# Performance work log

Hardware: AMD Instinct MI355X
Metric: run time of the kernel (lower is better)

Reference implementation:

```python
import jax, jax.numpy as jnp
import numpy as np

B = 8192
N_INPUTS = 16 * 12 * 64  # 12288, FEATURE_FACTORIZE=False
H0, H1, H2 = 256, 32, 32
OUTPUT_SCALE = 300.0
WDL_SCALE = 200.0
AVG_ACTIVE = 30.0  # ~30 active features per position (NNUE sparsity)


def setup_inputs() -> dict:
    key = jax.random.key(0)
    ks = jax.random.split(key, 11)
    p = AVG_ACTIVE / N_INPUTS
    # near-one-hot sparse binary feature vectors, as produced by get_features()
    wf = (jax.random.uniform(ks[0], (B, N_INPUTS)) < p).astype(jnp.float32)
    bf = (jax.random.uniform(ks[1], (B, N_INPUTS)) < p).astype(jnp.float32)
    side = jax.random.randint(ks[2], (B,), 0, 2).astype(jnp.bool_)
    qs1, qs2, qs3 = float(1 << 6), float(1 << 6), float(1 << 5)
    ft_w = jax.random.normal(ks[3], (H0, N_INPUTS), jnp.float32) * jnp.sqrt(2.0 / N_INPUTS)
    ft_b = jax.random.normal(ks[4], (H0,), jnp.float32) * 0.5
    l1_w = jax.random.normal(ks[5], (H1, 2 * H0), jnp.float32) * (32.0 / qs1)
    l1_b = jax.random.normal(ks[6], (H1,), jnp.float32) * 0.5
    l2_w = jax.random.normal(ks[7], (H2, H1), jnp.float32) * (32.0 / qs2)
    l2_b = jax.random.normal(ks[8], (H2,), jnp.float32) * 0.5
    l3_w = jax.random.normal(ks[9], (1, H2), jnp.float32) * (2048.0 / (OUTPUT_SCALE * qs3))
    l3_b = jax.random.normal(ks[10], (1,), jnp.float32) * 0.5
    return {"white_features": wf, "black_features": bf, "side": side,
            "ft_w": ft_w, "ft_b": ft_b, "l1_w": l1_w, "l1_b": l1_b,
            "l2_w": l2_w, "l2_b": l2_b, "l3_w": l3_w, "l3_b": l3_b}


def reference(white_features, black_features, side, ft_w, ft_b,
              l1_w, l1_b, l2_w, l2_b, l3_w, l3_b):
    # feature transformer on each perspective: [B, H0]
    w = white_features @ ft_w.T + ft_b
    b = black_features @ ft_w.T + ft_b
    s = side[:, None]
    # side-to-move perspective first: [B, 2*H0]
    acc = jnp.where(s, jnp.concatenate([w, b], axis=1),
                    jnp.concatenate([b, w], axis=1))
    o0 = jnp.clip(acc, 0.0, 1.0)
    o1 = jnp.clip(o0 @ l1_w.T + l1_b, 0.0, 1.0)
    o2 = jnp.clip(o1 @ l2_w.T + l2_b, 0.0, 1.0)
    o3 = (o2 @ l3_w.T + l3_b) * OUTPUT_SCALE  # [B, 1]
    return jax.nn.sigmoid(o3 / WDL_SCALE)
```

## Files before the change

kernel.cpp:

```cpp
#include <hip/hip_runtime.h>
#include <math.h>

#define NB 8192
#define NI 12288
#define H0 256
#define H1 32
#define H2 32
#define MAXA 256
#define OUT_SCALE 300.0f
#define WDL_SCALE 200.0f

typedef float f32x4 __attribute__((ext_vector_type(4)));

__global__ __launch_bounds__(256) void nnue_ft_transpose(
    const float* __restrict__ src, float* __restrict__ dst)
{
    __shared__ float tile[64][65];
    const int bx = blockIdx.x;
    const int by = blockIdx.y;
    const int tx = threadIdx.x;
    const int ty = threadIdx.y;
    const int col = bx * 64 + tx;
    for (int j = ty; j < 64; j += 4)
        tile[j][tx] = src[(size_t)(by * 64 + j) * NI + col];
    __syncthreads();
    const int h = by * 64 + tx;
    for (int j = ty; j < 64; j += 4)
        dst[(size_t)(bx * 64 + j) * H0 + h] = tile[tx][j];
}

__global__ __launch_bounds__(256) void nnue_fwd(
    const float* __restrict__ wf, const float* __restrict__ bf,
    const int* __restrict__ side,
    const float* __restrict__ ft,
    const float* __restrict__ ft_b,
    const float* __restrict__ l1_w, const float* __restrict__ l1_b,
    const float* __restrict__ l2_w, const float* __restrict__ l2_b,
    const float* __restrict__ l3_w, const float* __restrict__ l3_b,
    float* __restrict__ out, int tflag)
{
    __shared__ int   idxW[MAXA], idxB[MAXA];
    __shared__ int   cnts[2];
    __shared__ float o0[2 * H0];
    __shared__ float o1[H1];

    const int row = blockIdx.x;
    const int t   = threadIdx.x;
    if (t < 2) cnts[t] = 0;
    __syncthreads();

    const f32x4* wf4 = (const f32x4*)(wf + (size_t)row * NI);
    const f32x4* bf4 = (const f32x4*)(bf + (size_t)row * NI);
    const float ftb = ft_b[t];

    {
        f32x4 v[12];
        #pragma unroll
        for (int k = 0; k < 12; ++k)
            v[k] = __builtin_nontemporal_load(&wf4[t + k * 256]);
        #pragma unroll
        for (int k = 0; k < 12; ++k) {
            const int base = (t + k * 256) * 4;
            int m = (v[k].x != 0.f ? 1 : 0) | (v[k].y != 0.f ? 2 : 0)
                  | (v[k].z != 0.f ? 4 : 0) | (v[k].w != 0.f ? 8 : 0);
            while (m) {
                const int b = __ffs(m) - 1;
                m &= m - 1;
                idxW[atomicAdd(&cnts[0], 1)] = base + b;
            }
        }
    }
    {
        f32x4 v[12];
        #pragma unroll
        for (int k = 0; k < 12; ++k)
            v[k] = __builtin_nontemporal_load(&bf4[t + k * 256]);
        #pragma unroll
        for (int k = 0; k < 12; ++k) {
            const int base = (t + k * 256) * 4;
            int m = (v[k].x != 0.f ? 1 : 0) | (v[k].y != 0.f ? 2 : 0)
                  | (v[k].z != 0.f ? 4 : 0) | (v[k].w != 0.f ? 8 : 0);
            while (m) {
                const int b = __ffs(m) - 1;
                m &= m - 1;
                idxB[atomicAdd(&cnts[1], 1)] = base + b;
            }
        }
    }
    __syncthreads();

    const int nW = cnts[0], nB = cnts[1];
    float accW, accB;
    if (tflag) {
        float a0 = 0.f, a1 = 0.f, a2 = 0.f, a3 = 0.f;
        int i = 0;
        for (; i + 4 <= nW; i += 4) {
            const int i0 = __builtin_amdgcn_readfirstlane(idxW[i]);
            const int i1 = __builtin_amdgcn_readfirstlane(idxW[i + 1]);
            const int i2 = __builtin_amdgcn_readfirstlane(idxW[i + 2]);
            const int i3 = __builtin_amdgcn_readfirstlane(idxW[i + 3]);
            a0 += ft[(size_t)i0 * H0 + t];
            a1 += ft[(size_t)i1 * H0 + t];
            a2 += ft[(size_t)i2 * H0 + t];
            a3 += ft[(size_t)i3 * H0 + t];
        }
        for (; i < nW; ++i)
            a0 += ft[(size_t)__builtin_amdgcn_readfirstlane(idxW[i]) * H0 + t];
        accW = ftb + ((a0 + a1) + (a2 + a3));

        float b0 = 0.f, b1 = 0.f, b2 = 0.f, b3 = 0.f;
        i = 0;
        for (; i + 4 <= nB; i += 4) {
            const int i0 = __builtin_amdgcn_readfirstlane(idxB[i]);
            const int i1 = __builtin_amdgcn_readfirstlane(idxB[i + 1]);
            const int i2 = __builtin_amdgcn_readfirstlane(idxB[i + 2]);
            const int i3 = __builtin_amdgcn_readfirstlane(idxB[i + 3]);
            b0 += ft[(size_t)i0 * H0 + t];
            b1 += ft[(size_t)i1 * H0 + t];
            b2 += ft[(size_t)i2 * H0 + t];
            b3 += ft[(size_t)i3 * H0 + t];
        }
        for (; i < nB; ++i)
            b0 += ft[(size_t)__builtin_amdgcn_readfirstlane(idxB[i]) * H0 + t];
        accB = ftb + ((b0 + b1) + (b2 + b3));
    } else {
        accW = ftb; accB = ftb;
        const float* ftr = ft + (size_t)t * NI;
        for (int i = 0; i < nW; ++i) accW += ftr[idxW[i]];
        for (int i = 0; i < nB; ++i) accB += ftr[idxB[i]];
    }

    const bool s = side[row] != 0;
    const float wv = fminf(fmaxf(accW, 0.f), 1.f);
    const float bv = fminf(fmaxf(accB, 0.f), 1.f);
    o0[t]      = s ? wv : bv;
    o0[t + H0] = s ? bv : wv;
    __syncthreads();

    {
        const int j = t >> 3, p = t & 7;
        const float* wrow = l1_w + j * (2 * H0);
        float sum = 0.f;
        #pragma unroll
        for (int m = 0; m < 64; ++m) {
            const int k = p + 8 * m;
            sum += wrow[k] * o0[k];
        }
        sum += __shfl_xor(sum, 1);
        sum += __shfl_xor(sum, 2);
        sum += __shfl_xor(sum, 4);
        if (p == 0) o1[j] = fminf(fmaxf(sum + l1_b[j], 0.f), 1.f);
    }
    __syncthreads();

    if (t < 32) {
        const float* wrow = l2_w + t * H1;
        float sum2 = 0.f;
        #pragma unroll
        for (int k = 0; k < H1; ++k) sum2 += wrow[k] * o1[k];
        const float o2v = fminf(fmaxf(sum2 + l2_b[t], 0.f), 1.f);
        float part = o2v * l3_w[t];
        part += __shfl_xor(part, 1);
        part += __shfl_xor(part, 2);
        part += __shfl_xor(part, 4);
        part += __shfl_xor(part, 8);
        part += __shfl_xor(part, 16);
        if (t == 0) {
            const float o3 = (part + l3_b[0]) * OUT_SCALE;
            out[row] = 1.f / (1.f + __expf(-o3 / WDL_SCALE));
        }
    }
}

extern "C" void kernel_launch(void* const* d_in, const int* in_sizes, int n_in,
                              void* d_out, int out_size, void* d_ws, size_t ws_size,
                              hipStream_t stream) {
    const float* wf   = (const float*)d_in[0];
    const float* bf   = (const float*)d_in[1];
    const int*   side = (const int*)d_in[2];
    const float* ft_w = (const float*)d_in[3];
    const float* ft_b = (const float*)d_in[4];
    const float* l1_w = (const float*)d_in[5];
    const float* l1_b = (const float*)d_in[6];
    const float* l2_w = (const float*)d_in[7];
    const float* l2_b = (const float*)d_in[8];
    const float* l3_w = (const float*)d_in[9];
    const float* l3_b = (const float*)d_in[10];
    float*       out  = (float*)d_out;

    const size_t needT = (size_t)NI * H0 * sizeof(float);
    const int tflag = (ws_size >= needT) ? 1 : 0;
    const float* ft = ft_w;
    if (tflag) {
        float* ftT = (float*)d_ws;
        nnue_ft_transpose<<<dim3(NI / 64, H0 / 64), dim3(64, 4), 0, stream>>>(ft_w, ftT);
        ft = ftT;
    }
    nnue_fwd<<<NB, 256, 0, stream>>>(wf, bf, side, ft, ft_b,
                                     l1_w, l1_b, l2_w, l2_b, l3_w, l3_b,
                                     out, tflag);
}
```

Before: 183.4 us.

## Split sparse feature gather across wavefronts with vectorized row loads and LDS reduction

```diff
diff --git a/kernel.cpp b/kernel.cpp
--- a/kernel.cpp
+++ b/kernel.cpp
@@ -41,6 +41,7 @@
 {
     __shared__ int   idxW[MAXA], idxB[MAXA];
     __shared__ int   cnts[2];
+    __shared__ float pacc[4][2][H0] __attribute__((aligned(16)));
     __shared__ float o0[2 * H0];
     __shared__ float o1[H1];
 
@@ -90,46 +91,45 @@
     __syncthreads();
 
     const int nW = cnts[0], nB = cnts[1];
-    float accW, accB;
+    const int w = t >> 6;
+    const int l = t & 63;
+
     if (tflag) {
-        float a0 = 0.f, a1 = 0.f, a2 = 0.f, a3 = 0.f;
-        int i = 0;
-        for (; i + 4 <= nW; i += 4) {
-            const int i0 = __builtin_amdgcn_readfirstlane(idxW[i]);
-            const int i1 = __builtin_amdgcn_readfirstlane(idxW[i + 1]);
-            const int i2 = __builtin_amdgcn_readfirstlane(idxW[i + 2]);
-            const int i3 = __builtin_amdgcn_readfirstlane(idxW[i + 3]);
-            a0 += ft[(size_t)i0 * H0 + t];
-            a1 += ft[(size_t)i1 * H0 + t];
-            a2 += ft[(size_t)i2 * H0 + t];
-            a3 += ft[(size_t)i3 * H0 + t];
-        }
-        for (; i < nW; ++i)
-            a0 += ft[(size_t)__builtin_amdgcn_readfirstlane(idxW[i]) * H0 + t];
-        accW = ftb + ((a0 + a1) + (a2 + a3));
-
-        float b0 = 0.f, b1 = 0.f, b2 = 0.f, b3 = 0.f;
-        i = 0;
-        for (; i + 4 <= nB; i += 4) {
-            const int i0 = __builtin_amdgcn_readfirstlane(idxB[i]);
-            const int i1 = __builtin_amdgcn_readfirstlane(idxB[i + 1]);
-            const int i2 = __builtin_amdgcn_readfirstlane(idxB[i + 2]);
-            const int i3 = __builtin_amdgcn_readfirstlane(idxB[i + 3]);
-            b0 += ft[(size_t)i0 * H0 + t];
-            b1 += ft[(size_t)i1 * H0 + t];
-            b2 += ft[(size_t)i2 * H0 + t];
-            b3 += ft[(size_t)i3 * H0 + t];
-        }
-        for (; i < nB; ++i)
-            b0 += ft[(size_t)__builtin_amdgcn_readfirstlane(idxB[i]) * H0 + t];
-        accB = ftb + ((b0 + b1) + (b2 + b3));
+        f32x4 aw0 = {0.f, 0.f, 0.f, 0.f}, aw1 = {0.f, 0.f, 0.f, 0.f};
+        int i = w;
+        for (; i + 4 < nW; i += 8) {
+            const f32x4 r0 = *(const f32x4*)(ft + (size_t)idxW[i] * H0 + 4 * l);
+            const f32x4 r1 = *(const f32x4*)(ft + (size_t)idxW[i + 4] * H0 + 4 * l);
+            aw0 += r0; aw1 += r1;
+        }
+        if (i < nW)
+            aw0 += *(const f32x4*)(ft + (size_t)idxW[i] * H0 + 4 * l);
+
+        f32x4 ab0 = {0.f, 0.f, 0.f, 0.f}, ab1 = {0.f, 0.f, 0.f, 0.f};
+        i = w;
+        for (; i + 4 < nB; i += 8) {
+            const f32x4 r0 = *(const f32x4*)(ft + (size_t)idxB[i] * H0 + 4 * l);
+            const f32x4 r1 = *(const f32x4*)(ft + (size_t)idxB[i + 4] * H0 + 4 * l);
+            ab0 += r0; ab1 += r1;
+        }
+        if (i < nB)
+            ab0 += *(const f32x4*)(ft + (size_t)idxB[i] * H0 + 4 * l);
+
+        *(f32x4*)&pacc[w][0][4 * l] = aw0 + aw1;
+        *(f32x4*)&pacc[w][1][4 * l] = ab0 + ab1;
     } else {
-        accW = ftb; accB = ftb;
+        float aW = 0.f, aB = 0.f;
         const float* ftr = ft + (size_t)t * NI;
-        for (int i = 0; i < nW; ++i) accW += ftr[idxW[i]];
-        for (int i = 0; i < nB; ++i) accB += ftr[idxB[i]];
-    }
-
+        for (int j = 0; j < nW; ++j) aW += ftr[idxW[j]];
+        for (int j = 0; j < nB; ++j) aB += ftr[idxB[j]];
+        if (w == 0) { pacc[0][0][t % 64] = 0.f; }
+        pacc[0][0][t] = aW; pacc[1][0][t] = 0.f; pacc[2][0][t] = 0.f; pacc[3][0][t] = 0.f;
+        pacc[0][1][t] = aB; pacc[1][1][t] = 0.f; pacc[2][1][t] = 0.f; pacc[3][1][t] = 0.f;
+    }
+    __syncthreads();
+
+    const float accW = ftb + ((pacc[0][0][t] + pacc[1][0][t]) + (pacc[2][0][t] + pacc[3][0][t]));
+    const float accB = ftb + ((pacc[0][1][t] + pacc[1][1][t]) + (pacc[2][1][t] + pacc[3][1][t]));
     const bool s = side[row] != 0;
     const float wv = fminf(fmaxf(accW, 0.f), 1.f);
     const float bv = fminf(fmaxf(accB, 0.f), 1.f);
```

New measurement: 177.3 us. 3.3% less time.

## Process one batch row per wavefront with vectorized gather and transposed dense weights

Applied to the files above, without the earlier changes.

```diff
diff --git a/kernel.cpp b/kernel.cpp
--- a/kernel.cpp
+++ b/kernel.cpp
@@ -11,6 +11,11 @@
 #define WDL_SCALE 200.0f
 
 typedef float f32x4 __attribute__((ext_vector_type(4)));
+
+#define FTT_B  ((size_t)NI * H0 * 4)
+#define L1T_B  ((size_t)2 * H0 * H1 * 4)
+#define L2T_B  ((size_t)H1 * H2 * 4)
+#define WS_NEED (FTT_B + L1T_B + L2T_B)
 
 __global__ __launch_bounds__(256) void nnue_ft_transpose(
     const float* __restrict__ src, float* __restrict__ dst)
@@ -29,7 +34,167 @@
         dst[(size_t)(bx * 64 + j) * H0 + h] = tile[tx][j];
 }
 
-__global__ __launch_bounds__(256) void nnue_fwd(
+__global__ __launch_bounds__(256) void nnue_small_transpose(
+    const float* __restrict__ l1_w, const float* __restrict__ l2_w,
+    float* __restrict__ l1T, float* __restrict__ l2T)
+{
+    const int i = blockIdx.x * 256 + threadIdx.x;
+    if (i < 2 * H0 * H1) {
+        const int k = i >> 5, j = i & 31;
+        l1T[i] = l1_w[j * (2 * H0) + k];
+    }
+    const int i2 = i - 2 * H0 * H1;
+    if (i2 >= 0 && i2 < H1 * H2) {
+        const int k = i2 >> 5, j = i2 & 31;
+        l2T[i2] = l2_w[j * H1 + k];
+    }
+}
+
+__global__ __launch_bounds__(256) void nnue_fwd_wave(
+    const float* __restrict__ wf, const float* __restrict__ bf,
+    const int* __restrict__ side,
+    const float* __restrict__ ft,
+    const float* __restrict__ ft_b,
+    const float* __restrict__ l1T, const float* __restrict__ l1_b,
+    const float* __restrict__ l2T, const float* __restrict__ l2_b,
+    const float* __restrict__ l3_w, const float* __restrict__ l3_b,
+    float* __restrict__ out)
+{
+    __shared__ int   idx[4][2][MAXA];
+    __shared__ int   cnt[4][2];
+    __shared__ float o0s[4][2 * H0];
+    __shared__ float o1s[4][H1];
+
+    const int t = threadIdx.x;
+    const int w = t >> 6;
+    const int l = t & 63;
+    const int row = blockIdx.x * 4 + w;
+
+    if (l == 0) { cnt[w][0] = 0; cnt[w][1] = 0; }
+
+    #pragma unroll 1
+    for (int p = 0; p < 2; ++p) {
+        const float* src = p ? bf : wf;
+        const f32x4* s4 = (const f32x4*)(src + (size_t)row * NI);
+        int* myidx = idx[w][p];
+        int* mycnt = &cnt[w][p];
+
+        auto proc = [&](const f32x4* v, int cbase) {
+            #pragma unroll
+            for (int u = 0; u < 8; ++u) {
+                const int e = cbase * 512 + u * 64 + l;
+                int m = (v[u].x != 0.f ? 1 : 0) | (v[u].y != 0.f ? 2 : 0)
+                      | (v[u].z != 0.f ? 4 : 0) | (v[u].w != 0.f ? 8 : 0);
+                while (m) {
+                    const int b = __ffs(m) - 1;
+                    m &= m - 1;
+                    const int off = atomicAdd(mycnt, 1);
+                    if (off < MAXA) myidx[off] = e * 4 + b;
+                }
+            }
+        };
+
+        f32x4 va[8], vb[8];
+        #pragma unroll
+        for (int u = 0; u < 8; ++u)
+            va[u] = __builtin_nontemporal_load(&s4[u * 64 + l]);
+        #pragma unroll
+        for (int c = 0; c < 6; c += 2) {
+            #pragma unroll
+            for (int u = 0; u < 8; ++u)
+                vb[u] = __builtin_nontemporal_load(&s4[(c + 1) * 512 + u * 64 + l]);
+            proc(va, c);
+            if (c + 2 < 6) {
+                #pragma unroll
+                for (int u = 0; u < 8; ++u)
+                    va[u] = __builtin_nontemporal_load(&s4[(c + 2) * 512 + u * 64 + l]);
+            }
+            proc(vb, c + 1);
+        }
+    }
+
+    const int nW = min(cnt[w][0], MAXA);
+    const int nB = min(cnt[w][1], MAXA);
+    const float* ftl = ft + 4 * l;
+
+    f32x4 a0 = {0.f,0.f,0.f,0.f}, a1 = a0, a2 = a0, a3 = a0;
+    int i = 0;
+    for (; i + 4 <= nW; i += 4) {
+        const int i0 = __builtin_amdgcn_readfirstlane(idx[w][0][i]);
+        const int i1 = __builtin_amdgcn_readfirstlane(idx[w][0][i + 1]);
+        const int i2 = __builtin_amdgcn_readfirstlane(idx[w][0][i + 2]);
+        const int i3 = __builtin_amdgcn_readfirstlane(idx[w][0][i + 3]);
+        a0 += *(const f32x4*)(ftl + (size_t)i0 * H0);
+        a1 += *(const f32x4*)(ftl + (size_t)i1 * H0);
+        a2 += *(const f32x4*)(ftl + (size_t)i2 * H0);
+        a3 += *(const f32x4*)(ftl + (size_t)i3 * H0);
+    }
+    for (; i < nW; ++i)
+        a0 += *(const f32x4*)(ftl + (size_t)__builtin_amdgcn_readfirstlane(idx[w][0][i]) * H0);
+    f32x4 accW = (a0 + a1) + (a2 + a3);
+
+    f32x4 b0 = {0.f,0.f,0.f,0.f}, b1 = b0, b2 = b0, b3 = b0;
+    i = 0;
+    for (; i + 4 <= nB; i += 4) {
+        const int i0 = __builtin_amdgcn_readfirstlane(idx[w][1][i]);
+        const int i1 = __builtin_amdgcn_readfirstlane(idx[w][1][i + 1]);
+        const int i2 = __builtin_amdgcn_readfirstlane(idx[w][1][i + 2]);
+        const int i3 = __builtin_amdgcn_readfirstlane(idx[w][1][i + 3]);
+        b0 += *(const f32x4*)(ftl + (size_t)i0 * H0);
+        b1 += *(const f32x4*)(ftl + (size_t)i1 * H0);
+        b2 += *(const f32x4*)(ftl + (size_t)i2 * H0);
+        b3 += *(const f32x4*)(ftl + (size_t)i3 * H0);
+    }
+    for (; i < nB; ++i)
+        b0 += *(const f32x4*)(ftl + (size_t)__builtin_amdgcn_readfirstlane(idx[w][1][i]) * H0);
+    f32x4 accB = (b0 + b1) + (b2 + b3);
+
+    const f32x4 ftb4 = *(const f32x4*)(ft_b + 4 * l);
+    accW += ftb4;
+    accB += ftb4;
+    f32x4 wc, bc;
+    wc.x = fminf(fmaxf(accW.x, 0.f), 1.f); wc.y = fminf(fmaxf(accW.y, 0.f), 1.f);
+    wc.z = fminf(fmaxf(accW.z, 0.f), 1.f); wc.w = fminf(fmaxf(accW.w, 0.f), 1.f);
+    bc.x = fminf(fmaxf(accB.x, 0.f), 1.f); bc.y = fminf(fmaxf(accB.y, 0.f), 1.f);
+    bc.z = fminf(fmaxf(accB.z, 0.f), 1.f); bc.w = fminf(fmaxf(accB.w, 0.f), 1.f);
+    const bool s = side[row] != 0;
+    float* oseg = o0s[w];
+    *(f32x4*)&oseg[(s ? 0 : H0) + 4 * l] = wc;
+    *(f32x4*)&oseg[(s ? H0 : 0) + 4 * l] = bc;
+
+    {
+        const int j = l & 31, ph = l >> 5;
+        const float* l1c = l1T + (ph * 256) * 32 + j;
+        const float* ob  = oseg + ph * 256;
+        float sum = 0.f;
+        #pragma unroll 8
+        for (int m2 = 0; m2 < 256; ++m2)
+            sum += l1c[m2 * 32] * ob[m2];
+        sum += __shfl_xor(sum, 32);
+        if (l < 32)
+            o1s[w][l] = fminf(fmaxf(sum + l1_b[l], 0.f), 1.f);
+    }
+
+    if (l < 32) {
+        const float* l2c = l2T + l;
+        float s2 = 0.f;
+        #pragma unroll
+        for (int k = 0; k < H1; ++k) s2 += l2c[k * 32] * o1s[w][k];
+        const float o2v = fminf(fmaxf(s2 + l2_b[l], 0.f), 1.f);
+        float part = o2v * l3_w[l];
+        part += __shfl_xor(part, 1);
+        part += __shfl_xor(part, 2);
+        part += __shfl_xor(part, 4);
+        part += __shfl_xor(part, 8);
+        part += __shfl_xor(part, 16);
+        if (l == 0) {
+            const float o3 = (part + l3_b[0]) * OUT_SCALE;
+            out[row] = 1.f / (1.f + __expf(-o3 / WDL_SCALE));
+        }
+    }
+}
+
+__global__ __launch_bounds__(256) void nnue_fused_fallback(
     const float* __restrict__ wf, const float* __restrict__ bf,
     const int* __restrict__ side,
     const float* __restrict__ ft,
@@ -37,7 +202,7 @@
     const float* __restrict__ l1_w, const float* __restrict__ l1_b,
     const float* __restrict__ l2_w, const float* __restrict__ l2_b,
     const float* __restrict__ l3_w, const float* __restrict__ l3_b,
-    float* __restrict__ out, int tflag)
+    float* __restrict__ out)
 {
     __shared__ int   idxW[MAXA], idxB[MAXA];
     __shared__ int   cnts[2];
@@ -53,11 +218,13 @@
     const f32x4* bf4 = (const f32x4*)(bf + (size_t)row * NI);
     const float ftb = ft_b[t];
 
-    {
+    for (int half = 0; half < 2; ++half) {
+        const f32x4* p4 = half ? bf4 : wf4;
+        int* lst = half ? idxB : idxW;
         f32x4 v[12];
         #pragma unroll
         for (int k = 0; k < 12; ++k)
-            v[k] = __builtin_nontemporal_load(&wf4[t + k * 256]);
+            v[k] = __builtin_nontemporal_load(&p4[t + k * 256]);
         #pragma unroll
         for (int k = 0; k < 12; ++k) {
             const int base = (t + k * 256) * 4;
@@ -66,69 +233,17 @@
             while (m) {
                 const int b = __ffs(m) - 1;
                 m &= m - 1;
-                idxW[atomicAdd(&cnts[0], 1)] = base + b;
+                lst[atomicAdd(&cnts[half], 1)] = base + b;
             }
         }
     }
-    {
-        f32x4 v[12];
-        #pragma unroll
-        for (int k = 0; k < 12; ++k)
-            v[k] = __builtin_nontemporal_load(&bf4[t + k * 256]);
-        #pragma unroll
-        for (int k = 0; k < 12; ++k) {
-            const int base = (t + k * 256) * 4;
-            int m = (v[k].x != 0.f ? 1 : 0) | (v[k].y != 0.f ? 2 : 0)
-                  | (v[k].z != 0.f ? 4 : 0) | (v[k].w != 0.f ? 8 : 0);
-            while (m) {
-                const int b = __ffs(m) - 1;
-                m &= m - 1;
-                idxB[atomicAdd(&cnts[1], 1)] = base + b;
-            }
-        }
-    }
     __syncthreads();
 
     const int nW = cnts[0], nB = cnts[1];
-    float accW, accB;
-    if (tflag) {
-        float a0 = 0.f, a1 = 0.f, a2 = 0.f, a3 = 0.f;
-        int i = 0;
-        for (; i + 4 <= nW; i += 4) {
-            const int i0 = __builtin_amdgcn_readfirstlane(idxW[i]);
-            const int i1 = __builtin_amdgcn_readfirstlane(idxW[i + 1]);
-            const int i2 = __builtin_amdgcn_readfirstlane(idxW[i + 2]);
-            const int i3 = __builtin_amdgcn_readfirstlane(idxW[i + 3]);
-            a0 += ft[(size_t)i0 * H0 + t];
-            a1 += ft[(size_t)i1 * H0 + t];
-            a2 += ft[(size_t)i2 * H0 + t];
-            a3 += ft[(size_t)i3 * H0 + t];
-        }
-        for (; i < nW; ++i)
-            a0 += ft[(size_t)__builtin_amdgcn_readfirstlane(idxW[i]) * H0 + t];
-        accW = ftb + ((a0 + a1) + (a2 + a3));
-
-        float b0 = 0.f, b1 = 0.f, b2 = 0.f, b3 = 0.f;
-        i = 0;
-        for (; i + 4 <= nB; i += 4) {
-            const int i0 = __builtin_amdgcn_readfirstlane(idxB[i]);
-            const int i1 = __builtin_amdgcn_readfirstlane(idxB[i + 1]);
-            const int i2 = __builtin_amdgcn_readfirstlane(idxB[i + 2]);
-            const int i3 = __builtin_amdgcn_readfirstlane(idxB[i + 3]);
-            b0 += ft[(size_t)i0 * H0 + t];
-            b1 += ft[(size_t)i1 * H0 + t];
-            b2 += ft[(size_t)i2 * H0 + t];
-            b3 += ft[(size_t)i3 * H0 + t];
-        }
-        for (; i < nB; ++i)
-            b0 += ft[(size_t)__builtin_amdgcn_readfirstlane(idxB[i]) * H0 + t];
-        accB = ftb + ((b0 + b1) + (b2 + b3));
-    } else {
-        accW = ftb; accB = ftb;
-        const float* ftr = ft + (size_t)t * NI;
-        for (int i = 0; i < nW; ++i) accW += ftr[idxW[i]];
-        for (int i = 0; i < nB; ++i) accB += ftr[idxB[i]];
-    }
+    float accW = ftb, accB = ftb;
+    const float* ftr = ft + (size_t)t * NI;
+    for (int j = 0; j < nW; ++j) accW += ftr[idxW[j]];
+    for (int j = 0; j < nB; ++j) accB += ftr[idxB[j]];
 
     const bool s = side[row] != 0;
     const float wv = fminf(fmaxf(accW, 0.f), 1.f);
@@ -142,10 +257,7 @@
         const float* wrow = l1_w + j * (2 * H0);
         float sum = 0.f;
         #pragma unroll
-        for (int m = 0; m < 64; ++m) {
-            const int k = p + 8 * m;
-            sum += wrow[k] * o0[k];
-        }
+        for (int m = 0; m < 64; ++m) sum += wrow[p + 8 * m] * o0[p + 8 * m];
         sum += __shfl_xor(sum, 1);
         sum += __shfl_xor(sum, 2);
         sum += __shfl_xor(sum, 4);
@@ -188,15 +300,20 @@
     const float* l3_b = (const float*)d_in[10];
     float*       out  = (float*)d_out;
 
-    const size_t needT = (size_t)NI * H0 * sizeof(float);
-    const int tflag = (ws_size >= needT) ? 1 : 0;
-    const float* ft = ft_w;
-    if (tflag) {
+    if (ws_size >= WS_NEED) {
         float* ftT = (float*)d_ws;
+        float* l1T = (float*)((char*)d_ws + FTT_B);
+        float* l2T = (float*)((char*)d_ws + FTT_B + L1T_B);
+
         nnue_ft_transpose<<<dim3(NI / 64, H0 / 64), dim3(64, 4), 0, stream>>>(ft_w, ftT);
-        ft = ftT;
-    }
-    nnue_fwd<<<NB, 256, 0, stream>>>(wf, bf, side, ft, ft_b,
-                                     l1_w, l1_b, l2_w, l2_b, l3_w, l3_b,
-                                     out, tflag);
-}
+        nnue_small_transpose<<<(2 * H0 * H1 + H1 * H2 + 255) / 256, 256, 0, stream>>>(
+            l1_w, l2_w, l1T, l2T);
+        nnue_fwd_wave<<<NB / 4, 256, 0, stream>>>(wf, bf, side, ftT, ft_b,
+                                                  l1T, l1_b, l2T, l2_b,
+                                                  l3_w, l3_b, out);
+    } else {
+        nnue_fused_fallback<<<NB, 256, 0, stream>>>(wf, bf, side, ft_w, ft_b,
+                                                    l1_w, l1_b, l2_w, l2_b,
+                                                    l3_w, l3_b, out);
+    }
+}
```

Result: slower. 196.3 us (+7.0%).
